# Performance work log

Measured on AMD Instinct MI355X. Metric: run time of the kernel, lower is better.

Reference implementation:

```python
import jax, jax.numpy as jnp
import numpy as np


def setup_inputs() -> dict:
    key = jax.random.key(0)
    ks = jax.random.split(key, 8)
    B, P, K, N = 8, 16384, 16384, 16
    IN, REL, OUT = 64, 3, 64
    return {
        "keys": jax.random.normal(ks[0], (B, K, REL), dtype=jnp.float32),
        "points": jax.random.normal(ks[1], (B, P, REL), dtype=jnp.float32),
        "feats": jax.random.normal(ks[2], (B, P, IN), dtype=jnp.float32),
        "n_idxs": jax.random.randint(ks[3], (B, K, N), 0, P, dtype=jnp.int32),
        "neighbor_rel": jax.random.normal(ks[4], (B, K, N, REL), dtype=jnp.float32),
        "neighbor_valid": jax.random.randint(ks[5], (B, K, N), 0, 2, dtype=jnp.int32),
        "W": jax.random.normal(ks[6], (OUT, IN + REL), dtype=jnp.float32) / np.sqrt(IN + REL),
        "b": jax.random.normal(ks[7], (OUT,), dtype=jnp.float32) * 0.01,
    }


def reference(keys, points, feats, n_idxs, neighbor_rel, neighbor_valid, W, b):
    # gather neighbor features: feats[b, n_idxs[b]] per batch -> [B, K, N, IN]
    neighbor_feats = jax.vmap(lambda f, i: f[i])(feats, n_idxs)
    comb = jnp.concatenate([neighbor_feats, neighbor_rel], axis=-1)  # [B,K,N,IN+REL]
    valid = neighbor_valid.astype(comb.dtype)                        # [B,K,N]
    cleared = comb * valid[..., None]
    counts = valid.sum(-1)                                           # [B,K]
    inv_counts = jnp.where(counts > 0, 1.0 / jnp.maximum(counts, 1.0), 0.0)
    sum_feats = cleared.sum(axis=2)                                  # [B,K,IN+REL]
    scaled = sum_feats * inv_counts[..., None]
    return jax.nn.relu(jnp.einsum('bkc,oc->bko', scaled, W) + b)
```

## Files before the change

kernel.cpp:

```cpp
#include <hip/hip_runtime.h>

#define BB   8
#define PP   16384
#define KK   16384
#define NN   16
#define CIN  64
#define REL  3
#define CC   67
#define OUTC 64
#define KPAD 96
#define PITCH_US 104
#define GPW  2


typedef short s16x8 __attribute__((ext_vector_type(8)));
typedef float f32x4 __attribute__((ext_vector_type(4)));

static __device__ __forceinline__ unsigned short bf16_rne(float f) {
    unsigned int u = __float_as_uint(f);
    u += 0x7FFF + ((u >> 16) & 1);
    return (unsigned short)(u >> 16);
}

__global__ __launch_bounds__(256, 4) void graphconv_kernel(
    const float* __restrict__ feats,
    const int*   __restrict__ n_idxs,
    const float* __restrict__ neighbor_rel,
    const int*   __restrict__ neighbor_valid,
    const float* __restrict__ Wm,
    const float* __restrict__ bvec,
    float*       __restrict__ out)
{
    __shared__ __align__(16) unsigned short Wbf[OUTC * PITCH_US];
    __shared__ __align__(16) unsigned short Stile[4 * 16 * PITCH_US];

    const int tid = threadIdx.x;

    {
        unsigned int* w32 = (unsigned int*)Wbf;
        for (int j = tid; j < OUTC * (PITCH_US / 2); j += 256) {
            const int o = j / (PITCH_US / 2);
            const int d = j - o * (PITCH_US / 2);
            const int c0 = 2 * d, c1 = 2 * d + 1;
            const float w0 = (c0 < CC) ? Wm[o * CC + c0] : 0.0f;
            const float w1 = (c1 < CC) ? Wm[o * CC + c1] : 0.0f;
            w32[j] = (unsigned int)bf16_rne(w0) |
                     ((unsigned int)bf16_rne(w1) << 16);
        }
    }
    __syncthreads();

    const int lane = tid & 63;
    const int wave = __builtin_amdgcn_readfirstlane(tid >> 6);
    unsigned short* Sw = &Stile[wave * 16 * PITCH_US];

    {
        unsigned int* s32 = (unsigned int*)Sw;
        for (int j = lane; j < 16 * (PITCH_US / 2); j += 64) s32[j] = 0u;
    }

    s16x8 Bfr[4][3];
#pragma unroll
    for (int t = 0; t < 4; ++t)
#pragma unroll
        for (int q = 0; q < 3; ++q) {
            s16x8 v = *(const s16x8*)&Wbf[(t * 16 + (lane & 15)) * PITCH_US
                                          + q * 32 + (lane >> 4) * 8];
            asm volatile("" : "+v"(v));
            Bfr[t][q] = v;
        }
    float bias_t[4];
#pragma unroll
    for (int t = 0; t < 4; ++t) bias_t[t] = bvec[t * 16 + (lane & 15)];

    const int b   = blockIdx.x & 7;
    const int bib = blockIdx.x >> 3;
    const float* fb = feats + (size_t)b * ((size_t)PP * CIN);

    for (int g = 0; g < GPW; ++g) {
        const int kbase = ((bib * 4 + wave) * GPW + g) * 16;

        for (int i = 0; i < 16; ++i) {
            const size_t row  = (size_t)b * KK + (size_t)(kbase + i);
            const int*   idxp = n_idxs         + row * NN;
            const int*   vp   = neighbor_valid + row * NN;
            const float* relp = neighbor_rel   + row * (NN * REL);

            float sum = 0.0f, r0 = 0.0f, r1 = 0.0f, r2 = 0.0f;
            int count = 0;
#pragma unroll
            for (int n = 0; n < NN; ++n) {
                const int   v  = vp[n];
                const int   id = idxp[n];
                const float m  = (float)v;
                const float gv = fb[(size_t)id * CIN + lane];
                sum = fmaf(m, gv, sum);
                r0  = fmaf(m, relp[n * 3 + 0], r0);
                r1  = fmaf(m, relp[n * 3 + 1], r1);
                r2  = fmaf(m, relp[n * 3 + 2], r2);
                count += v;
            }
            const float inv = (count > 0) ? (1.0f / (float)count) : 0.0f;

            Sw[i * PITCH_US + lane] = bf16_rne(sum * inv);
            if (lane < 3) {
                const float rv = (lane == 0) ? r0 : ((lane == 1) ? r1 : r2);
                Sw[i * PITCH_US + 64 + lane] = bf16_rne(rv * inv);
            }
        }

        f32x4 C0 = {0.f,0.f,0.f,0.f}, C1 = {0.f,0.f,0.f,0.f};
        f32x4 C2 = {0.f,0.f,0.f,0.f}, C3 = {0.f,0.f,0.f,0.f};
#pragma unroll
        for (int q = 0; q < 3; ++q) {
            const s16x8 A = *(const s16x8*)&Sw[(lane & 15) * PITCH_US
                                               + q * 32 + (lane >> 4) * 8];
            C0 = __builtin_amdgcn_mfma_f32_16x16x32_bf16(A, Bfr[0][q], C0, 0, 0, 0);
            C1 = __builtin_amdgcn_mfma_f32_16x16x32_bf16(A, Bfr[1][q], C1, 0, 0, 0);
            C2 = __builtin_amdgcn_mfma_f32_16x16x32_bf16(A, Bfr[2][q], C2, 0, 0, 0);
            C3 = __builtin_amdgcn_mfma_f32_16x16x32_bf16(A, Bfr[3][q], C3, 0, 0, 0);
        }

        const int m0 = (lane >> 4) * 4;
        const int oc = lane & 15;
#pragma unroll
        for (int r = 0; r < 4; ++r) {
            const size_t orow = ((size_t)b * KK + (size_t)(kbase + m0 + r)) * OUTC;
            out[orow + 0  + oc] = fmaxf(C0[r] + bias_t[0], 0.0f);
            out[orow + 16 + oc] = fmaxf(C1[r] + bias_t[1], 0.0f);
            out[orow + 32 + oc] = fmaxf(C2[r] + bias_t[2], 0.0f);
            out[orow + 48 + oc] = fmaxf(C3[r] + bias_t[3], 0.0f);
        }
    }
}

extern "C" void kernel_launch(void* const* d_in, const int* in_sizes, int n_in,
                              void* d_out, int out_size, void* d_ws, size_t ws_size,
                              hipStream_t stream) {
    const float* feats = (const float*)d_in[2];
    const int*   nidx  = (const int*)  d_in[3];
    const float* nrel  = (const float*)d_in[4];
    const int*   nval  = (const int*)  d_in[5];
    const float* Wm    = (const float*)d_in[6];
    const float* bv    = (const float*)d_in[7];
    float* out = (float*)d_out;

    graphconv_kernel<<<dim3(1024), dim3(256), 0, stream>>>(
        feats, nidx, nrel, nval, Wm, bv, out);
}
```

Baseline: 173.8 us.

## Drop per-wave group loop, double grid, pair rows, load weights from LDS

Each wave now handles one 16-row group instead of two, and the grid is doubled to 2048 blocks. The weight fragments are read from LDS at MFMA time instead of being pinned in registers, and launch bounds are raised to 6 blocks per CU. The neighbor gather loop handles two rows at once so more independent loads are in flight. The aim is more occupancy and memory-level parallelism for the latency-bound gather. The cost is that twice as many blocks each redo the W bf16 conversion into LDS, and the extra per-block setup may offset the gain.

```diff
diff --git a/kernel.cpp b/kernel.cpp
--- a/kernel.cpp
+++ b/kernel.cpp
@@ -10,7 +10,6 @@
 #define OUTC 64
 #define KPAD 96
 #define PITCH_US 104
-#define GPW  2
 
 
 typedef short s16x8 __attribute__((ext_vector_type(8)));
@@ -22,7 +21,7 @@
     return (unsigned short)(u >> 16);
 }
 
-__global__ __launch_bounds__(256, 4) void graphconv_kernel(
+__global__ __launch_bounds__(256, 6) void graphconv_kernel(
     const float* __restrict__ feats,
     const int*   __restrict__ n_idxs,
     const float* __restrict__ neighbor_rel,
@@ -59,78 +58,86 @@
         for (int j = lane; j < 16 * (PITCH_US / 2); j += 64) s32[j] = 0u;
     }
 
-    s16x8 Bfr[4][3];
-#pragma unroll
-    for (int t = 0; t < 4; ++t)
-#pragma unroll
-        for (int q = 0; q < 3; ++q) {
-            s16x8 v = *(const s16x8*)&Wbf[(t * 16 + (lane & 15)) * PITCH_US
-                                          + q * 32 + (lane >> 4) * 8];
-            asm volatile("" : "+v"(v));
-            Bfr[t][q] = v;
-        }
-    float bias_t[4];
-#pragma unroll
-    for (int t = 0; t < 4; ++t) bias_t[t] = bvec[t * 16 + (lane & 15)];
-
     const int b   = blockIdx.x & 7;
     const int bib = blockIdx.x >> 3;
     const float* fb = feats + (size_t)b * ((size_t)PP * CIN);
 
-    for (int g = 0; g < GPW; ++g) {
-        const int kbase = ((bib * 4 + wave) * GPW + g) * 16;
+    const int kbase = (bib * 4 + wave) * 16;
 
-        for (int i = 0; i < 16; ++i) {
-            const size_t row  = (size_t)b * KK + (size_t)(kbase + i);
-            const int*   idxp = n_idxs         + row * NN;
-            const int*   vp   = neighbor_valid + row * NN;
-            const float* relp = neighbor_rel   + row * (NN * REL);
+    for (int ip = 0; ip < 8; ++ip) {
+        const int iA = 2 * ip, iB = 2 * ip + 1;
+        const size_t rowA = (size_t)b * KK + (size_t)(kbase + iA);
+        const size_t rowB = rowA + 1;
+        const int*   idxA = n_idxs         + rowA * NN;
+        const int*   idxB = n_idxs         + rowB * NN;
+        const int*   vpA  = neighbor_valid + rowA * NN;
+        const int*   vpB  = neighbor_valid + rowB * NN;
+        const float* relA = neighbor_rel   + rowA * (NN * REL);
+        const float* relB = neighbor_rel   + rowB * (NN * REL);
 
-            float sum = 0.0f, r0 = 0.0f, r1 = 0.0f, r2 = 0.0f;
-            int count = 0;
+        float sumA = 0.f, a0 = 0.f, a1 = 0.f, a2 = 0.f;
+        float sumB = 0.f, b0 = 0.f, b1 = 0.f, b2 = 0.f;
+        int cntA = 0, cntB = 0;
 #pragma unroll
-            for (int n = 0; n < NN; ++n) {
-                const int   v  = vp[n];
-                const int   id = idxp[n];
-                const float m  = (float)v;
-                const float gv = fb[(size_t)id * CIN + lane];
-                sum = fmaf(m, gv, sum);
-                r0  = fmaf(m, relp[n * 3 + 0], r0);
-                r1  = fmaf(m, relp[n * 3 + 1], r1);
-                r2  = fmaf(m, relp[n * 3 + 2], r2);
-                count += v;
-            }
-            const float inv = (count > 0) ? (1.0f / (float)count) : 0.0f;
+        for (int n = 0; n < NN; ++n) {
+            const int   vA = vpA[n],  vB = vpB[n];
+            const int   dA = idxA[n], dB = idxB[n];
+            const float mA = (float)vA, mB = (float)vB;
+            const float gA = fb[(size_t)dA * CIN + lane];
+            const float gB = fb[(size_t)dB * CIN + lane];
+            sumA = fmaf(mA, gA, sumA);
+            sumB = fmaf(mB, gB, sumB);
+            a0 = fmaf(mA, relA[n * 3 + 0], a0);
+            a1 = fmaf(mA, relA[n * 3 + 1], a1);
+            a2 = fmaf(mA, relA[n * 3 + 2], a2);
+            b0 = fmaf(mB, relB[n * 3 + 0], b0);
+            b1 = fmaf(mB, relB[n * 3 + 1], b1);
+            b2 = fmaf(mB, relB[n * 3 + 2], b2);
+            cntA += vA; cntB += vB;
+        }
+        const float invA = (cntA > 0) ? (1.0f / (float)cntA) : 0.0f;
+        const float invB = (cntB > 0) ? (1.0f / (float)cntB) : 0.0f;
 
-            Sw[i * PITCH_US + lane] = bf16_rne(sum * inv);
-            if (lane < 3) {
-                const float rv = (lane == 0) ? r0 : ((lane == 1) ? r1 : r2);
-                Sw[i * PITCH_US + 64 + lane] = bf16_rne(rv * inv);
-            }
+        Sw[iA * PITCH_US + lane] = bf16_rne(sumA * invA);
+        Sw[iB * PITCH_US + lane] = bf16_rne(sumB * invB);
+        if (lane < 3) {
+            const float rA = (lane == 0) ? a0 : ((lane == 1) ? a1 : a2);
+            const float rB = (lane == 0) ? b0 : ((lane == 1) ? b1 : b2);
+            Sw[iA * PITCH_US + 64 + lane] = bf16_rne(rA * invA);
+            Sw[iB * PITCH_US + 64 + lane] = bf16_rne(rB * invB);
         }
+    }
 
-        f32x4 C0 = {0.f,0.f,0.f,0.f}, C1 = {0.f,0.f,0.f,0.f};
-        f32x4 C2 = {0.f,0.f,0.f,0.f}, C3 = {0.f,0.f,0.f,0.f};
+    f32x4 C0 = {0.f,0.f,0.f,0.f}, C1 = {0.f,0.f,0.f,0.f};
+    f32x4 C2 = {0.f,0.f,0.f,0.f}, C3 = {0.f,0.f,0.f,0.f};
 #pragma unroll
-        for (int q = 0; q < 3; ++q) {
-            const s16x8 A = *(const s16x8*)&Sw[(lane & 15) * PITCH_US
-                                               + q * 32 + (lane >> 4) * 8];
-            C0 = __builtin_amdgcn_mfma_f32_16x16x32_bf16(A, Bfr[0][q], C0, 0, 0, 0);
-            C1 = __builtin_amdgcn_mfma_f32_16x16x32_bf16(A, Bfr[1][q], C1, 0, 0, 0);
-            C2 = __builtin_amdgcn_mfma_f32_16x16x32_bf16(A, Bfr[2][q], C2, 0, 0, 0);
-            C3 = __builtin_amdgcn_mfma_f32_16x16x32_bf16(A, Bfr[3][q], C3, 0, 0, 0);
-        }
+    for (int q = 0; q < 3; ++q) {
+        const s16x8 A = *(const s16x8*)&Sw[(lane & 15) * PITCH_US
+                                           + q * 32 + (lane >> 4) * 8];
+        const int ko = q * 32 + (lane >> 4) * 8;
+        const s16x8 B0 = *(const s16x8*)&Wbf[( 0 + (lane & 15)) * PITCH_US + ko];
+        const s16x8 B1 = *(const s16x8*)&Wbf[(16 + (lane & 15)) * PITCH_US + ko];
+        const s16x8 B2 = *(const s16x8*)&Wbf[(32 + (lane & 15)) * PITCH_US + ko];
+        const s16x8 B3 = *(const s16x8*)&Wbf[(48 + (lane & 15)) * PITCH_US + ko];
+        C0 = __builtin_amdgcn_mfma_f32_16x16x32_bf16(A, B0, C0, 0, 0, 0);
+        C1 = __builtin_amdgcn_mfma_f32_16x16x32_bf16(A, B1, C1, 0, 0, 0);
+        C2 = __builtin_amdgcn_mfma_f32_16x16x32_bf16(A, B2, C2, 0, 0, 0);
+        C3 = __builtin_amdgcn_mfma_f32_16x16x32_bf16(A, B3, C3, 0, 0, 0);
+    }
 
-        const int m0 = (lane >> 4) * 4;
-        const int oc = lane & 15;
+    const float bias0 = bvec[ 0 + (lane & 15)];
+    const float bias1 = bvec[16 + (lane & 15)];
+    const float bias2 = bvec[32 + (lane & 15)];
+    const float bias3 = bvec[48 + (lane & 15)];
+    const int m0 = (lane >> 4) * 4;
+    const int oc = lane & 15;
 #pragma unroll
-        for (int r = 0; r < 4; ++r) {
-            const size_t orow = ((size_t)b * KK + (size_t)(kbase + m0 + r)) * OUTC;
-            out[orow + 0  + oc] = fmaxf(C0[r] + bias_t[0], 0.0f);
-            out[orow + 16 + oc] = fmaxf(C1[r] + bias_t[1], 0.0f);
-            out[orow + 32 + oc] = fmaxf(C2[r] + bias_t[2], 0.0f);
-            out[orow + 48 + oc] = fmaxf(C3[r] + bias_t[3], 0.0f);
-        }
+    for (int r = 0; r < 4; ++r) {
+        const size_t orow = ((size_t)b * KK + (size_t)(kbase + m0 + r)) * OUTC;
+        out[orow + 0  + oc] = fmaxf(C0[r] + bias0, 0.0f);
+        out[orow + 16 + oc] = fmaxf(C1[r] + bias1, 0.0f);
+        out[orow + 32 + oc] = fmaxf(C2[r] + bias2, 0.0f);
+        out[orow + 48 + oc] = fmaxf(C3[r] + bias3, 0.0f);
     }
 }
 
@@ -145,6 +152,6 @@
     const float* bv    = (const float*)d_in[7];
     float* out = (float*)d_out;
 
-    graphconv_kernel<<<dim3(1024), dim3(256), 0, stream>>>(
+    graphconv_kernel<<<dim3(2048), dim3(256), 0, stream>>>(
         feats, nidx, nrel, nval, Wm, bv, out);
 }
```

After: 183.7 us. +5.7%, slower.
